# Kernel optimization log

Measured on AMD Instinct MI355X. Metric: run time of the kernel, lower is better.

## Reference

```python
import jax, jax.numpy as jnp
import numpy as np

N = 50000      # nodes
E = 800000     # edges (avg degree 16)
DIM = 256      # in_channels == heads * out_channels
H = 8          # heads
C = DIM // H   # per-head out_channels = 32
EDGE_DIM = 2
NEG_SLOPE = 0.2


def setup_inputs() -> dict:
    key = jax.random.key(0)
    ks = jax.random.split(key, 8)
    x = jax.random.normal(ks[0], (N, DIM), dtype=jnp.float32)
    edge_index = jax.random.randint(ks[1], (2, E), 0, N, dtype=jnp.int32)
    edge_attr = jax.random.normal(ks[2], (E, EDGE_DIM), dtype=jnp.float32)
    s = 1.0 / np.sqrt(DIM)
    W_l = jax.random.normal(ks[3], (DIM, H * C), dtype=jnp.float32) * s   # lin_l (src)
    W_r = jax.random.normal(ks[4], (DIM, H * C), dtype=jnp.float32) * s   # lin_r (dst)
    W_e = jax.random.normal(ks[5], (EDGE_DIM, H * C), dtype=jnp.float32) * (1.0 / np.sqrt(EDGE_DIM))
    att = jax.random.normal(ks[6], (H, C), dtype=jnp.float32) * s         # attention vector a
    bias = jnp.zeros((H * C,), dtype=jnp.float32)
    return {"x": x, "edge_index": edge_index, "edge_attr": edge_attr,
            "W_l": W_l, "W_r": W_r, "W_e": W_e, "att": att, "bias": bias}


def reference(x, edge_index, edge_attr, W_l, W_r, W_e, att, bias):
    src, dst = edge_index[0], edge_index[1]
    # --- add self loops; fill_value='mean' => scatter-mean of incoming edge_attr per node ---
    attr_sum = jax.ops.segment_sum(edge_attr, dst, num_segments=N)          # [N, 2]
    cnt = jax.ops.segment_sum(jnp.ones((edge_attr.shape[0], 1), edge_attr.dtype), dst, num_segments=N)
    loop_attr = attr_sum / jnp.maximum(cnt, 1.0)                             # [N, 2], 0 for isolated nodes
    idx = jnp.arange(N, dtype=src.dtype)
    src_a = jnp.concatenate([src, idx])                                      # [E+N]
    dst_a = jnp.concatenate([dst, idx])
    ea = jnp.concatenate([edge_attr, loop_attr], axis=0)                     # [E+N, 2]
    # --- GATv2: project src/dst/edge features ---
    x_l = (x @ W_l).reshape(N, H, C)
    x_r = (x @ W_r).reshape(N, H, C)
    e_e = (ea @ W_e).reshape(-1, H, C)                                       # [E+N, H, C]
    m = x_l[src_a] + x_r[dst_a] + e_e                                        # [E+N, H, C]
    score = jnp.einsum('ehc,hc->eh', jax.nn.leaky_relu(m, NEG_SLOPE), att)   # [E+N, H]
    # --- segment softmax over incoming edges of each dst (self loop guarantees >=1 edge) ---
    smax = jax.ops.segment_max(score, dst_a, num_segments=N)                 # [N, H]
    ex = jnp.exp(score - smax[dst_a])
    denom = jax.ops.segment_sum(ex, dst_a, num_segments=N)                   # [N, H]
    alpha = ex / denom[dst_a]                                                # [E+N, H]
    # --- weighted scatter-add of src messages ---
    out = jax.ops.segment_sum(alpha[..., None] * x_l[src_a], dst_a, num_segments=N)  # [N, H, C]
    return out.reshape(N, H * C) + bias
```

## Files before the change

### kernel.cpp

```cpp
#include <hip/hip_runtime.h>
#include <hip/hip_bf16.h>

#define NN 50000
#define NPAD 53248
#define EE 800000
#define DIM 256
#define NEG_SLOPE 0.2f
#define LOG2E 1.44269504088896f

#define GEMM_BLOCKS 1564
#define FILL_BLOCKS 3125
#define CNT_BLOCKS  3125
#define CVT_BLOCKS  12500
#define WT_BLOCKS   512

typedef __attribute__((ext_vector_type(8))) short short8;
typedef __attribute__((ext_vector_type(4))) float f32x4;

__device__ __forceinline__ unsigned short f2bf(float f) {
    unsigned u = __float_as_uint(f);
    unsigned r = (u + 0x7fffu + ((u >> 16) & 1u)) >> 16;
    return (unsigned short)r;
}
__device__ __forceinline__ float bf2f(unsigned short h) {
    return __uint_as_float(((unsigned)h) << 16);
}

__global__ __launch_bounds__(256) void k_prep_count(
    const float* __restrict__ x, const float* __restrict__ Wl,
    const float* __restrict__ Wr, const int* __restrict__ ei,
    unsigned short* __restrict__ xb, unsigned short* __restrict__ wt,
    int* __restrict__ cnt, int* __restrict__ rank)
{
    int b = blockIdx.x;
    if (b < CNT_BLOCKS) {
        int e = b * 256 + threadIdx.x;
        if (e < EE) {
            int dst = ei[EE + e];
            rank[e] = atomicAdd(&cnt[dst], 1);
        }
    } else if (b < CNT_BLOCKS + CVT_BLOCKS) {
        int i = ((b - CNT_BLOCKS) * 256 + threadIdx.x) * 4;
        float4 v = *(const float4*)(x + i);
        ushort4 o;
        o.x = f2bf(v.x); o.y = f2bf(v.y); o.z = f2bf(v.z); o.w = f2bf(v.w);
        *(ushort4*)(xb + i) = o;
    } else {
        int idx = (b - CNT_BLOCKS - CVT_BLOCKS) * 256 + threadIdx.x;
        int n = idx >> 8, k = idx & 255;
        float v = (n < 256) ? Wl[k * 256 + n] : Wr[k * 256 + (n - 256)];
        wt[idx] = f2bf(v);
    }
}

__global__ __launch_bounds__(1024) void k_scan(
    const int* __restrict__ cnt, int* __restrict__ row_start)
{
    __shared__ int wsum[16];
    int tid = threadIdx.x, lane = tid & 63, wid = tid >> 6;
    int carry = 0;
    for (int base = 0; base < NPAD; base += 4096) {
        int idx = base + tid * 4;
        int4 v = *(const int4*)(cnt + idx);
        int tsum = v.x + v.y + v.z + v.w;
        int s = tsum;
#pragma unroll
        for (int off = 1; off < 64; off <<= 1) {
            int t = __shfl_up(s, off, 64);
            if (lane >= off) s += t;
        }
        if (lane == 63) wsum[wid] = s;
        __syncthreads();
        int wpre = 0, tot = 0;
#pragma unroll
        for (int w = 0; w < 16; ++w) {
            int xv = wsum[w];
            tot += xv;
            if (w < wid) wpre += xv;
        }
        int ex = carry + wpre + (s - tsum);
        int4 o;
        o.x = ex;
        o.y = o.x + v.x;
        o.z = o.y + v.y;
        o.w = o.z + v.z;
        *(int4*)(row_start + idx) = o;
        carry += tot;
        __syncthreads();
    }
}

__global__ __launch_bounds__(256) void k_gemm_fill(
    const unsigned short* __restrict__ xb, const unsigned short* __restrict__ wt,
    const int* __restrict__ ei, const float* __restrict__ ea,
    const int* __restrict__ row_start, const int* __restrict__ rank,
    unsigned short* __restrict__ xlr, uint2* __restrict__ edge_rec)
{
    __shared__ short sAB[8192];
    int tid = threadIdx.x;

    if (blockIdx.x >= GEMM_BLOCKS) {
        int e = (blockIdx.x - GEMM_BLOCKS) * 256 + tid;
        if (e < EE) {
            int src = ei[e];
            int dst = ei[EE + e];
            float2 a = *(const float2*)(ea + 2 * e);
            int pos = row_start[dst] + rank[e];
            unsigned packed = ((unsigned)f2bf(a.y) << 16) | f2bf(a.x);
            edge_rec[pos] = make_uint2((unsigned)src, packed);
        }
        return;
    }

    int wid = tid >> 6, lane = tid & 63;
    int mt = blockIdx.x >> 2, nt = blockIdx.x & 3;
    int mBase = mt * 128, nBase = nt * 128;
    int wm = (wid & 1) * 64, wn = (wid >> 1) * 64;
    int q = lane >> 4, mh = lane & 15;

    f32x4 acc[4][4];
#pragma unroll
    for (int i = 0; i < 4; ++i)
#pragma unroll
        for (int j = 0; j < 4; ++j)
            acc[i][j] = (f32x4){0.f, 0.f, 0.f, 0.f};

    int aoff[4], boff[4];
#pragma unroll
    for (int f = 0; f < 4; ++f) {
        int r  = wm + f * 16 + mh;
        aoff[f] = (r * 4 + (q ^ (r & 3))) * 8;
        int nl = wn + f * 16 + mh;
        boff[f] = 4096 + (nl * 4 + (q ^ (nl & 3))) * 8;
    }

    for (int k0 = 0; k0 < 256; k0 += 32) {
        __syncthreads();
#pragma unroll
        for (int it = 0; it < 4; ++it) {
            int L = it * 256 + tid;
            const unsigned short* g;
            if (L < 512) {
                int r  = L >> 2;
                int qq = (L & 3) ^ (r & 3);
                int grow = mBase + r;
                if (grow > NN - 1) grow = NN - 1;
                g = xb + (size_t)grow * 256 + k0 + qq * 8;
            } else {
                int LB = L - 512;
                int nl = LB >> 2;
                int qq = (LB & 3) ^ (nl & 3);
                g = wt + (size_t)(nBase + nl) * 256 + k0 + qq * 8;
            }
            short* lp = sAB + (it * 256 + wid * 64) * 8;
            __builtin_amdgcn_global_load_lds(
                (const __attribute__((address_space(1))) void*)g,
                (__attribute__((address_space(3))) void*)lp, 16, 0, 0);
        }
        __syncthreads();

        short8 af[4], bfr[4];
#pragma unroll
        for (int f = 0; f < 4; ++f) af[f]  = *(const short8*)(sAB + aoff[f]);
#pragma unroll
        for (int f = 0; f < 4; ++f) bfr[f] = *(const short8*)(sAB + boff[f]);
#pragma unroll
        for (int i = 0; i < 4; ++i)
#pragma unroll
            for (int j = 0; j < 4; ++j)
                acc[i][j] = __builtin_amdgcn_mfma_f32_16x16x32_bf16(
                    af[i], bfr[j], acc[i][j], 0, 0, 0);
    }

#pragma unroll
    for (int i = 0; i < 4; ++i)
#pragma unroll
        for (int j = 0; j < 4; ++j)
#pragma unroll
            for (int r = 0; r < 4; ++r) {
                int row = mBase + wm + i * 16 + q * 4 + r;
                if (row < NN) {
                    int col = nBase + wn + j * 16 + mh;
                    xlr[(size_t)row * 512 + col] = f2bf(acc[i][j][r]);
                }
            }
}

__global__ __launch_bounds__(256) void k_attn(
    const unsigned short* __restrict__ xlr, const int* __restrict__ row_start,
    const uint2* __restrict__ edge_rec, const float* __restrict__ W_e,
    const float* __restrict__ att, const float* __restrict__ bias,
    float* __restrict__ out)
{
    int n = __builtin_amdgcn_readfirstlane(blockIdx.x * 4 + (threadIdx.x >> 6));
    if (n >= NN) return;
    int lane = threadIdx.x & 63;
    int j = lane * 4;

    const unsigned short* nrow = xlr + ((size_t)n << 9);
    ushort4 xru = *(const ushort4*)(nrow + 256 + j);
    float4 xr4 = make_float4(bf2f(xru.x), bf2f(xru.y), bf2f(xru.z), bf2f(xru.w));
    float4 att4 = *(const float4*)(att + j);
    att4.x *= LOG2E; att4.y *= LOG2E; att4.z *= LOG2E; att4.w *= LOG2E;
    float4 a02  = make_float4(att4.x * NEG_SLOPE, att4.y * NEG_SLOPE,
                              att4.z * NEG_SLOPE, att4.w * NEG_SLOPE);
    float4 we0  = *(const float4*)(W_e + j);
    float4 we1  = *(const float4*)(W_e + 256 + j);

    int rs = __builtin_amdgcn_readfirstlane(row_start[n]);
    int cn = __builtin_amdgcn_readfirstlane(row_start[n + 1]) - rs;

    float D = 0.0f, la0 = 0.0f, la1 = 0.0f;
    float4 acc = make_float4(0.f, 0.f, 0.f, 0.f);

    auto process = [&](ushort4 xu, float a0, float a1) {
        float4 xl4 = make_float4(bf2f(xu.x), bf2f(xu.y), bf2f(xu.z), bf2f(xu.w));
        float m0 = fmaf(a0, we0.x, fmaf(a1, we1.x, xl4.x + xr4.x));
        float m1 = fmaf(a0, we0.y, fmaf(a1, we1.y, xl4.y + xr4.y));
        float m2 = fmaf(a0, we0.z, fmaf(a1, we1.z, xl4.z + xr4.z));
        float m3 = fmaf(a0, we0.w, fmaf(a1, we1.w, xl4.w + xr4.w));
        float p0 = (m0 > 0.f) ? att4.x : a02.x;
        float p1 = (m1 > 0.f) ? att4.y : a02.y;
        float p2 = (m2 > 0.f) ? att4.z : a02.z;
        float p3 = (m3 > 0.f) ? att4.w : a02.w;
        float s = fmaf(m0, p0, fmaf(m1, p1, fmaf(m2, p2, m3 * p3)));
        s += __shfl_xor(s, 1, 64);
        s += __shfl_xor(s, 2, 64);
        s += __shfl_xor(s, 4, 64);
        float w = __builtin_amdgcn_exp2f(s);
        D += w;
        acc.x = fmaf(w, xl4.x, acc.x);
        acc.y = fmaf(w, xl4.y, acc.y);
        acc.z = fmaf(w, xl4.z, acc.z);
        acc.w = fmaf(w, xl4.w, acc.w);
    };

    if (cn > 0) {
        uint2 r0 = edge_rec[rs];
        uint2 r1 = (cn > 1) ? edge_rec[rs + 1] : r0;
        uint2 r2 = (cn > 2) ? edge_rec[rs + 2] : r1;
        int s0 = __builtin_amdgcn_readfirstlane((int)r0.x);
        ushort4 x0 = *(const ushort4*)(xlr + ((size_t)s0 << 9) + j);
        int s1 = __builtin_amdgcn_readfirstlane((int)r1.x);
        ushort4 x1 = *(const ushort4*)(xlr + ((size_t)s1 << 9) + j);
        for (int i = 0; i < cn; ++i) {
            int i3 = (i + 3 < cn) ? i + 3 : cn - 1;
            uint2 r3 = edge_rec[rs + i3];
            int s2 = __builtin_amdgcn_readfirstlane((int)r2.x);
            ushort4 x2 = *(const ushort4*)(xlr + ((size_t)s2 << 9) + j);
            float a0 = __uint_as_float(r0.y << 16);
            float a1 = __uint_as_float(r0.y & 0xffff0000u);
            la0 += a0;
            la1 += a1;
            process(x0, a0, a1);
            r0 = r1; r1 = r2; r2 = r3;
            x0 = x1; x1 = x2;
        }
    }
    float invc = 1.0f / fmaxf((float)cn, 1.0f);
    ushort4 xs = *(const ushort4*)(nrow + j);
    process(xs, la0 * invc, la1 * invc);

    float invD = 1.0f / D;
    float4 b4 = *(const float4*)(bias + j);
    float4 o;
    o.x = fmaf(acc.x, invD, b4.x);
    o.y = fmaf(acc.y, invD, b4.y);
    o.z = fmaf(acc.z, invD, b4.z);
    o.w = fmaf(acc.w, invD, b4.w);
    *(float4*)(out + (size_t)n * 256 + j) = o;
}

extern "C" void kernel_launch(void* const* d_in, const int* in_sizes, int n_in,
                              void* d_out, int out_size, void* d_ws, size_t ws_size,
                              hipStream_t stream)
{
    const float* x    = (const float*)d_in[0];
    const int*   ei   = (const int*)  d_in[1];
    const float* ea   = (const float*)d_in[2];
    const float* Wl   = (const float*)d_in[3];
    const float* Wr   = (const float*)d_in[4];
    const float* We   = (const float*)d_in[5];
    const float* att  = (const float*)d_in[6];
    const float* bias = (const float*)d_in[7];
    float* out = (float*)d_out;

    char* ws = (char*)d_ws;
    size_t off = 0;
    unsigned short* xlr = (unsigned short*)(ws + off); off += (size_t)NN * 512 * 2;
    unsigned short* xb  = (unsigned short*)(ws + off); off += (size_t)NN * 256 * 2;
    uint2*  edge_rec    = (uint2*)(ws + off);          off += (size_t)EE * 8;
    int*    rank        = (int*)(ws + off);            off += (size_t)EE * 4;
    unsigned short* wt  = (unsigned short*)(ws + off); off += (size_t)512 * 256 * 2;
    int*    cnt         = (int*)(ws + off);            off += (size_t)NPAD * 4;
    int*    row_st      = (int*)(ws + off);            off += (size_t)NPAD * 4;

    hipMemsetAsync(cnt, 0, NPAD * sizeof(int), stream);

    k_prep_count<<<CNT_BLOCKS + CVT_BLOCKS + WT_BLOCKS, 256, 0, stream>>>(
        x, Wl, Wr, ei, xb, wt, cnt, rank);
    k_scan      <<<1, 1024, 0, stream>>>(cnt, row_st);
    k_gemm_fill <<<GEMM_BLOCKS + FILL_BLOCKS, 256, 0, stream>>>(
        xb, wt, ei, ea, row_st, rank, xlr, edge_rec);
    k_attn      <<<12500, 256, 0, stream>>>(
        xlr, row_st, edge_rec, We, att, bias, out);
}
```

Before: 299.9 us.

## Batch edge-record loads per wave, use DPP reductions, preload scan inputs

In the attention kernel, each wave now loads up to 64 edge records in one coalesced load and pulls each source index and attribute with readlane, instead of issuing a dependent scalar-broadcast load per edge. The source-row gathers are software-pipelined four deep. The per-head 8-lane score reduction uses DPP row operations in place of shfl_xor, which cuts LDS/permute traffic. The scan kernel preloads all 13 count chunks into registers before the serial scan. The edge record buffer is padded and zeroed so the lane loads stay in bounds, which adds a small memset.

```diff
diff --git a/kernel.cpp b/kernel.cpp
--- a/kernel.cpp
+++ b/kernel.cpp
@@ -24,6 +24,17 @@
 }
 __device__ __forceinline__ float bf2f(unsigned short h) {
     return __uint_as_float(((unsigned)h) << 16);
+}
+
+__device__ __forceinline__ float red8(float s) {
+    int t;
+    t = __builtin_amdgcn_update_dpp(0, __float_as_int(s), 0xB1, 0xF, 0xF, true);
+    s += __int_as_float(t);
+    t = __builtin_amdgcn_update_dpp(0, __float_as_int(s), 0x4E, 0xF, 0xF, true);
+    s += __int_as_float(t);
+    t = __builtin_amdgcn_update_dpp(0, __float_as_int(s), 0x141, 0xF, 0xF, true);
+    s += __int_as_float(t);
+    return s;
 }
 
 __global__ __launch_bounds__(256) void k_prep_count(
@@ -58,11 +69,15 @@
 {
     __shared__ int wsum[16];
     int tid = threadIdx.x, lane = tid & 63, wid = tid >> 6;
+    int4 v[13];
+#pragma unroll
+    for (int p = 0; p < 13; ++p)
+        v[p] = *(const int4*)(cnt + p * 4096 + tid * 4);
     int carry = 0;
-    for (int base = 0; base < NPAD; base += 4096) {
-        int idx = base + tid * 4;
-        int4 v = *(const int4*)(cnt + idx);
-        int tsum = v.x + v.y + v.z + v.w;
+#pragma unroll
+    for (int p = 0; p < 13; ++p) {
+        int4 vv = v[p];
+        int tsum = vv.x + vv.y + vv.z + vv.w;
         int s = tsum;
 #pragma unroll
         for (int off = 1; off < 64; off <<= 1) {
@@ -81,10 +96,10 @@
         int ex = carry + wpre + (s - tsum);
         int4 o;
         o.x = ex;
-        o.y = o.x + v.x;
-        o.z = o.y + v.y;
-        o.w = o.z + v.z;
-        *(int4*)(row_start + idx) = o;
+        o.y = o.x + vv.x;
+        o.z = o.y + vv.y;
+        o.w = o.z + vv.z;
+        *(int4*)(row_start + p * 4096 + tid * 4) = o;
         carry += tot;
         __syncthreads();
     }
@@ -213,7 +228,7 @@
     float D = 0.0f, la0 = 0.0f, la1 = 0.0f;
     float4 acc = make_float4(0.f, 0.f, 0.f, 0.f);
 
-    auto process = [&](ushort4 xu, float a0, float a1) {
+    auto body = [&](ushort4 xu, float a0, float a1) {
         float4 xl4 = make_float4(bf2f(xu.x), bf2f(xu.y), bf2f(xu.z), bf2f(xu.w));
         float m0 = fmaf(a0, we0.x, fmaf(a1, we1.x, xl4.x + xr4.x));
         float m1 = fmaf(a0, we0.y, fmaf(a1, we1.y, xl4.y + xr4.y));
@@ -224,9 +239,7 @@
         float p2 = (m2 > 0.f) ? att4.z : a02.z;
         float p3 = (m3 > 0.f) ? att4.w : a02.w;
         float s = fmaf(m0, p0, fmaf(m1, p1, fmaf(m2, p2, m3 * p3)));
-        s += __shfl_xor(s, 1, 64);
-        s += __shfl_xor(s, 2, 64);
-        s += __shfl_xor(s, 4, 64);
+        s = red8(s);
         float w = __builtin_amdgcn_exp2f(s);
         D += w;
         acc.x = fmaf(w, xl4.x, acc.x);
@@ -235,31 +248,40 @@
         acc.w = fmaf(w, xl4.w, acc.w);
     };
 
-    if (cn > 0) {
-        uint2 r0 = edge_rec[rs];
-        uint2 r1 = (cn > 1) ? edge_rec[rs + 1] : r0;
-        uint2 r2 = (cn > 2) ? edge_rec[rs + 2] : r1;
-        int s0 = __builtin_amdgcn_readfirstlane((int)r0.x);
-        ushort4 x0 = *(const ushort4*)(xlr + ((size_t)s0 << 9) + j);
-        int s1 = __builtin_amdgcn_readfirstlane((int)r1.x);
-        ushort4 x1 = *(const ushort4*)(xlr + ((size_t)s1 << 9) + j);
-        for (int i = 0; i < cn; ++i) {
-            int i3 = (i + 3 < cn) ? i + 3 : cn - 1;
-            uint2 r3 = edge_rec[rs + i3];
-            int s2 = __builtin_amdgcn_readfirstlane((int)r2.x);
-            ushort4 x2 = *(const ushort4*)(xlr + ((size_t)s2 << 9) + j);
-            float a0 = __uint_as_float(r0.y << 16);
-            float a1 = __uint_as_float(r0.y & 0xffff0000u);
-            la0 += a0;
-            la1 += a1;
-            process(x0, a0, a1);
-            r0 = r1; r1 = r2; r2 = r3;
-            x0 = x1; x1 = x2;
-        }
-    }
+    int done = 0;
+    while (done < cn) {
+        int m = cn - done; if (m > 64) m = 64;
+        int ridx = rs + done + lane;
+        if (ridx > EE + 63) ridx = EE + 63;
+        uint2 rc = edge_rec[ridx];
+        int rcx = (int)rc.x, rca = (int)rc.y;
+
+        auto gat = [&](int k) -> ushort4 {
+            unsigned sidx = (unsigned)__builtin_amdgcn_readlane(rcx, k);
+            return *(const ushort4*)(xlr + ((size_t)sidx << 9) + j);
+        };
+        auto proc = [&](ushort4 xu, int k) {
+            unsigned pk = (unsigned)__builtin_amdgcn_readlane(rca, k);
+            float a0 = __uint_as_float(pk << 16);
+            float a1 = __uint_as_float(pk & 0xffff0000u);
+            la0 += a0; la1 += a1;
+            body(xu, a0, a1);
+        };
+
+        ushort4 x0 = gat(0), x1 = gat(1), x2 = gat(2), x3 = gat(3);
+        for (int i = 0; i < m; i += 4) {
+            proc(x0, i);
+            if (i + 4 < m) x0 = gat(i + 4);
+            if (i + 1 < m) { proc(x1, i + 1); if (i + 5 < m) x1 = gat(i + 5); }
+            if (i + 2 < m) { proc(x2, i + 2); if (i + 6 < m) x2 = gat(i + 6); }
+            if (i + 3 < m) { proc(x3, i + 3); if (i + 7 < m) x3 = gat(i + 7); }
+        }
+        done += m;
+    }
+
     float invc = 1.0f / fmaxf((float)cn, 1.0f);
     ushort4 xs = *(const ushort4*)(nrow + j);
-    process(xs, la0 * invc, la1 * invc);
+    body(xs, la0 * invc, la1 * invc);
 
     float invD = 1.0f / D;
     float4 b4 = *(const float4*)(bias + j);
@@ -289,13 +311,14 @@
     size_t off = 0;
     unsigned short* xlr = (unsigned short*)(ws + off); off += (size_t)NN * 512 * 2;
     unsigned short* xb  = (unsigned short*)(ws + off); off += (size_t)NN * 256 * 2;
-    uint2*  edge_rec    = (uint2*)(ws + off);          off += (size_t)EE * 8;
+    uint2*  edge_rec    = (uint2*)(ws + off);          off += (size_t)(EE + 64) * 8;
     int*    rank        = (int*)(ws + off);            off += (size_t)EE * 4;
     unsigned short* wt  = (unsigned short*)(ws + off); off += (size_t)512 * 256 * 2;
     int*    cnt         = (int*)(ws + off);            off += (size_t)NPAD * 4;
     int*    row_st      = (int*)(ws + off);            off += (size_t)NPAD * 4;
 
     hipMemsetAsync(cnt, 0, NPAD * sizeof(int), stream);
+    hipMemsetAsync(edge_rec + EE, 0, 64 * sizeof(uint2), stream);
 
     k_prep_count<<<CNT_BLOCKS + CVT_BLOCKS + WT_BLOCKS, 256, 0, stream>>>(
         x, Wl, Wr, ei, xb, wt, cnt, rank);
```

New measurement: 276.5 us. 1.08x faster.
